# Kernel optimization log

Measured on AMD Instinct MI355X. Metric: run time of the kernel, lower is better.

Reference implementation:

```python
import jax, jax.numpy as jnp
import numpy as np

D_IN, D_HID, N_TOK = 2048, 8192, 8192

def _ternary(key, shape):
    # ternary {-1, 0, 1} weights stored as float32
    return jax.random.randint(key, shape, -1, 2).astype(jnp.float32)

def setup_inputs() -> dict:
    key = jax.random.key(0)
    kx, k1, k2, kh, k3 = jax.random.split(key, 5)
    return {
        "x": jax.random.normal(kx, (N_TOK, D_IN), dtype=jnp.float32),
        "W1": _ternary(k1, (D_HID, D_IN)),   # gate proj
        "W2": _ternary(k2, (D_HID, D_IN)),   # value proj
        "Wh": _ternary(kh, (D_HID, D_HID)),  # hidden layer (depth-1 == 1)
        "W3": _ternary(k3, (D_IN, D_HID)),   # output proj
        # per-layer dequant scales (scalar), ~1/sqrt(fan_in)
        "s1": jnp.float32(1.0 / np.sqrt(D_IN)),
        "s2": jnp.float32(1.0 / np.sqrt(D_IN)),
        "sh": jnp.float32(1.0 / np.sqrt(D_HID)),
        "s3": jnp.float32(1.0 / np.sqrt(D_HID)),
    }

def _tlin(x, W, s):
    # ternary packed linear: dequantized matmul, no bias
    return jnp.einsum('td,hd->th', x, W) * s

def reference(x, W1, W2, Wh, W3, s1, s2, sh, s3):
    h = jax.nn.silu(_tlin(x, W1, s1)) * _tlin(x, W2, s2)   # SwiGLU entry
    h = jax.nn.gelu(_tlin(h, Wh, sh), approximate=False)    # hidden block (depth-1)
    return _tlin(h, W3, s3)                                 # [N_TOK, D_IN]
```

## Files before the change

### kernel.cpp

```cpp
#include <hip/hip_runtime.h>
#include <hip/hip_bf16.h>
#include <stdint.h>

typedef __bf16 bf16;
typedef __bf16 bf16x8 __attribute__((ext_vector_type(8)));
typedef float f32x4 __attribute__((ext_vector_type(4)));

typedef uint32_t __attribute__((address_space(1))) * gptr_as1;
typedef uint32_t __attribute__((address_space(3))) * lptr_as3;

__device__ __forceinline__ void async16(const void* g, void* l) {
    __builtin_amdgcn_global_load_lds((gptr_as1)(uintptr_t)g,
                                     (lptr_as3)(uintptr_t)l,
                                     16, 0, 0);
}

__device__ __forceinline__ void bar() {
    asm volatile("" ::: "memory");
    __builtin_amdgcn_s_barrier();
    asm volatile("" ::: "memory");
}

__global__ void cvt_f32_bf16_kernel(const float* __restrict__ src,
                                    bf16* __restrict__ dst, int n8) {
    int i = blockIdx.x * blockDim.x + threadIdx.x;
    if (i >= n8) return;
    const float4* s = reinterpret_cast<const float4*>(src);
    float4 a = s[2 * (size_t)i], b = s[2 * (size_t)i + 1];
    bf16x8 v;
    v[0] = (bf16)a.x; v[1] = (bf16)a.y; v[2] = (bf16)a.z; v[3] = (bf16)a.w;
    v[4] = (bf16)b.x; v[5] = (bf16)b.y; v[6] = (bf16)b.z; v[7] = (bf16)b.w;
    *reinterpret_cast<bf16x8*>(dst + (size_t)i * 8) = v;
}

__global__ void cvt_ilv_kernel(const float* __restrict__ src,
                               bf16* __restrict__ dst, int n8, int sel) {
    int i = blockIdx.x * blockDim.x + threadIdx.x;
    if (i >= n8) return;
    const int row = i >> 8;
    const int c = i & 255;
    const int drow = ((row >> 4) << 5) + (sel << 4) + (row & 15);
    const float4* s = reinterpret_cast<const float4*>(src);
    float4 a = s[2 * (size_t)i], b = s[2 * (size_t)i + 1];
    bf16x8 v;
    v[0] = (bf16)a.x; v[1] = (bf16)a.y; v[2] = (bf16)a.z; v[3] = (bf16)a.w;
    v[4] = (bf16)b.x; v[5] = (bf16)b.y; v[6] = (bf16)b.z; v[7] = (bf16)b.w;
    *reinterpret_cast<bf16x8*>(dst + ((size_t)drow * 256 + c) * 8) = v;
}

template <int EPI, int K>
__global__ __launch_bounds__(256, 2)
void gemm2t(const bf16* __restrict__ A, const bf16* __restrict__ B,
            void* __restrict__ Cout, const float* __restrict__ s1p,
            const float* __restrict__ s2p, int N, int ldh) {
    __shared__ __align__(16) char sm[49152];

    const int tid = threadIdx.x;
    const int w = tid >> 6, l = tid & 63;
    const int wr = w >> 1, wc = w & 1;

    const int gx = gridDim.x;
    const int nwg = gx * (int)gridDim.y;
    const int orig = blockIdx.y * gx + blockIdx.x;
    const int wg = (orig & 7) * (nwg >> 3) + (orig >> 3);
    const int bm = wg / gx, bn = wg % gx;

    constexpr int NT = K / 32;

    f32x4 acc[8][4] = {};

    const int arow = bm * 256, brow = bn * 128;

    const int sr = l >> 2;
    const int sg = ((l & 3) ^ ((l >> 3) & 3)) << 4;
    const char* qa0 = (const char*)(A + (size_t)(arow +   0 + w * 16 + sr) * K) + sg;
    const char* qa1 = (const char*)(A + (size_t)(arow +  64 + w * 16 + sr) * K) + sg;
    const char* qa2 = (const char*)(A + (size_t)(arow + 128 + w * 16 + sr) * K) + sg;
    const char* qa3 = (const char*)(A + (size_t)(arow + 192 + w * 16 + sr) * K) + sg;
    const char* qb0 = (const char*)(B + (size_t)(brow +   0 + w * 16 + sr) * K) + sg;
    const char* qb1 = (const char*)(B + (size_t)(brow +  64 + w * 16 + sr) * K) + sg;
    const int ldw = w * 1024;

    auto STAGE_TILE = [&](int p) {
        char* ba = sm + p * 24576;
        char* bb = ba + 16384;
        async16(qa0, ba +     0 + ldw); async16(qa1, ba +  4096 + ldw);
        async16(qa2, ba +  8192 + ldw); async16(qa3, ba + 12288 + ldw);
        async16(qb0, bb +     0 + ldw); async16(qb1, bb +  4096 + ldw);
    };
    auto ADV = [&]() {
        qa0 += 64; qa1 += 64; qa2 += 64; qa3 += 64; qb0 += 64; qb1 += 64;
    };

    const int rlane = l & 15;
    const int chi = (l >> 4) << 4;

    STAGE_TILE(0);
    ADV();
    asm volatile("s_waitcnt vmcnt(0)" ::: "memory");
    bar();

#pragma unroll 1
    for (int kt = 0; kt < NT; ++kt) {
        if (kt + 1 < NT) { STAGE_TILE((kt + 1) & 1); ADV(); }
        const char* ba = sm + (kt & 1) * 24576;
        const char* bb = ba + 16384;

        bf16x8 av[8], bv[4];
#pragma unroll
        for (int i = 0; i < 8; ++i) {
            const int row = wr * 128 + i * 16 + rlane;
            av[i] = *reinterpret_cast<const bf16x8*>(
                ba + row * 64 + (chi ^ (((row >> 1) & 3) << 4)));
        }
#pragma unroll
        for (int j = 0; j < 4; ++j) {
            const int row = wc * 64 + j * 16 + rlane;
            bv[j] = *reinterpret_cast<const bf16x8*>(
                bb + row * 64 + (chi ^ (((row >> 1) & 3) << 4)));
        }
        asm volatile("s_waitcnt lgkmcnt(0)" ::: "memory");
        __builtin_amdgcn_sched_barrier(0);
        __builtin_amdgcn_s_setprio(1);
#pragma unroll
        for (int i = 0; i < 8; ++i)
#pragma unroll
            for (int j = 0; j < 4; ++j)
                acc[i][j] = __builtin_amdgcn_mfma_f32_16x16x32_bf16(av[i], bv[j], acc[i][j], 0, 0, 0);
        __builtin_amdgcn_s_setprio(0);
        asm volatile("s_waitcnt vmcnt(0)" ::: "memory");
        bar();
    }

    const float s1 = s1p[0];
    const int r0 = bm * 256 + wr * 128 + ((l >> 4) << 2);
    if constexpr (EPI == 2) {
        const float s2 = s2p[0];
        const int hcb = (bn * 4 + wc * 2) * 16 + rlane;
#pragma unroll
        for (int i = 0; i < 8; ++i)
#pragma unroll
            for (int jp = 0; jp < 2; ++jp)
#pragma unroll
                for (int q = 0; q < 4; ++q) {
                    float g = acc[i][2 * jp][q] * s1;
                    float v = acc[i][2 * jp + 1][q] * s2;
                    float sig = 1.0f / (1.0f + __expf(-g));
                    ((bf16*)Cout)[(size_t)(r0 + i * 16 + q) * ldh + hcb + jp * 16] =
                        (bf16)(g * sig * v);
                }
    } else {
        const int c0 = bn * 128 + wc * 64 + rlane;
#pragma unroll
        for (int i = 0; i < 8; ++i)
#pragma unroll
            for (int j = 0; j < 4; ++j)
#pragma unroll
                for (int q = 0; q < 4; ++q) {
                    float v = acc[i][j][q] * s1;
                    size_t idx = (size_t)(r0 + i * 16 + q) * N + (c0 + j * 16);
                    if constexpr (EPI == 0) {
                        float g = 0.5f * v * (1.0f + erff(v * 0.70710678118654752f));
                        ((bf16*)Cout)[idx] = (bf16)g;
                    } else {
                        ((float*)Cout)[idx] = v;
                    }
                }
    }
}

template <int EPI, int K>
__global__ __launch_bounds__(512, 1)
void gemm8p(const bf16* __restrict__ A, const bf16* __restrict__ B,
            void* __restrict__ Cout, const float* __restrict__ s1p,
            const float* __restrict__ s2p, int N, int ldh) {
    __shared__ __align__(16) char sm[131072];

    const int tid = threadIdx.x;
    const int w = tid >> 6, l = tid & 63;
    const int wr = w >> 2, wc = w & 3;

    const int gx = gridDim.x;
    const int nwg = gx * (int)gridDim.y;
    const int orig = blockIdx.y * gx + blockIdx.x;
    const int wg = (orig & 7) * (nwg >> 3) + (orig >> 3);
    const int bm = wg / gx, bn = wg % gx;

    constexpr int NT = K / 64;

    f32x4 acc[8][4] = {};

    char* const bufA0 = sm;
    char* const bufB0 = sm + 32768;
    char* const bufA1 = sm + 65536;
    char* const bufB1 = sm + 98304;
    const int arow = bm * 256, brow = bn * 256;

    const int srow_in = l >> 3;
    const int scolb = ((l & 7) ^ srow_in) << 4;
    auto STAGE = [&](char* ldsT, const bf16* g, int grow0, int kt, int r0) {
        const int rr = r0 + w * 8 + srow_in;
        const char* gp = (const char*)(g + (size_t)(grow0 + rr) * K + kt * 64) + scolb;
        async16(gp, ldsT + r0 * 128 + w * 1024);
    };

    const int rlane = l & 15;
    const int chi = (l >> 4) << 4;
    const int sw = (rlane & 7) << 4;
    const int ksd = (rlane & 4) ? -64 : 64;
    const int offA = (wr * 128 + rlane) * 128 + (chi ^ sw);
    const int offB = (wc * 64 + rlane) * 128 + (chi ^ sw);
    const char* const pA0  = bufA0 + offA;  const char* const pA0k = pA0 + ksd;
    const char* const pB0  = bufB0 + offB;  const char* const pB0k = pB0 + ksd;
    const char* const pA1  = bufA1 + offA;  const char* const pA1k = pA1 + ksd;
    const char* const pB1  = bufB1 + offB;  const char* const pB1k = pB1 + ksd;

    STAGE(bufA0, A, arow, 0, 0);   STAGE(bufA0, A, arow, 0, 128);
    STAGE(bufB0, B, brow, 0, 0);   STAGE(bufB0, B, brow, 0, 64);
    STAGE(bufB0, B, brow, 0, 128); STAGE(bufB0, B, brow, 0, 192);
    STAGE(bufA0, A, arow, 0, 64);  STAGE(bufA0, A, arow, 0, 192);
    STAGE(bufA1, A, arow, 1, 0);   STAGE(bufA1, A, arow, 1, 128);
    STAGE(bufB1, B, brow, 1, 0);   STAGE(bufB1, B, brow, 1, 64);
    STAGE(bufB1, B, brow, 1, 128); STAGE(bufB1, B, brow, 1, 192);
    asm volatile("s_waitcnt vmcnt(6)" ::: "memory");
    bar();

    auto body = [&](int kt, char* cA, char* cB, char* nA,
                    const char* pa, const char* pak,
                    const char* pb, const char* pbk) {
        bf16x8 ae[4], ao[4], bv[4];
#pragma unroll
        for (int i = 0; i < 4; ++i)
            ae[i] = *reinterpret_cast<const bf16x8*>(pa + i * 2048);
#pragma unroll
        for (int j = 0; j < 4; ++j)
            bv[j] = *reinterpret_cast<const bf16x8*>(pb + j * 2048);
        if (kt + 1 < NT) { STAGE(nA, A, arow, kt + 1, 64); STAGE(nA, A, arow, kt + 1, 192); }
        bar();
        asm volatile("s_waitcnt lgkmcnt(0)" ::: "memory");
        __builtin_amdgcn_sched_barrier(0);
        __builtin_amdgcn_s_setprio(1);
#pragma unroll
        for (int i = 0; i < 4; ++i)
#pragma unroll
            for (int j = 0; j < 4; ++j)
                acc[i][j] = __builtin_amdgcn_mfma_f32_16x16x32_bf16(ae[i], bv[j], acc[i][j], 0, 0, 0);
        __builtin_amdgcn_s_setprio(0);
        bar();
#pragma unroll
        for (int i = 0; i < 4; ++i)
            ao[i] = *reinterpret_cast<const bf16x8*>(pa + 8192 + i * 2048);
        bar();
        asm volatile("s_waitcnt lgkmcnt(0)" ::: "memory");
        __builtin_amdgcn_sched_barrier(0);
        __builtin_amdgcn_s_setprio(1);
#pragma unroll
        for (int i = 0; i < 4; ++i)
#pragma unroll
            for (int j = 0; j < 4; ++j)
                acc[4 + i][j] = __builtin_amdgcn_mfma_f32_16x16x32_bf16(ao[i], bv[j], acc[4 + i][j], 0, 0, 0);
        __builtin_amdgcn_s_setprio(0);
        bar();
#pragma unroll
        for (int i = 0; i < 4; ++i)
            ae[i] = *reinterpret_cast<const bf16x8*>(pak + i * 2048);
#pragma unroll
        for (int j = 0; j < 4; ++j)
            bv[j] = *reinterpret_cast<const bf16x8*>(pbk + j * 2048);
        if (kt + 2 < NT) { STAGE(cB, B, brow, kt + 2, 0); STAGE(cB, B, brow, kt + 2, 64); }
        bar();
        asm volatile("s_waitcnt lgkmcnt(0)" ::: "memory");
        __builtin_amdgcn_sched_barrier(0);
        __builtin_amdgcn_s_setprio(1);
#pragma unroll
        for (int i = 0; i < 4; ++i)
#pragma unroll
            for (int j = 0; j < 4; ++j)
                acc[i][j] = __builtin_amdgcn_mfma_f32_16x16x32_bf16(ae[i], bv[j], acc[i][j], 0, 0, 0);
        __builtin_amdgcn_s_setprio(0);
        bar();
#pragma unroll
        for (int i = 0; i < 4; ++i)
            ao[i] = *reinterpret_cast<const bf16x8*>(pak + 8192 + i * 2048);
        if (kt + 2 < NT) {
            STAGE(cB, B, brow, kt + 2, 128); STAGE(cB, B, brow, kt + 2, 192);
            STAGE(cA, A, arow, kt + 2, 0);   STAGE(cA, A, arow, kt + 2, 128);
        }
        bar();
        asm volatile("s_waitcnt lgkmcnt(0)" ::: "memory");
        __builtin_amdgcn_sched_barrier(0);
        __builtin_amdgcn_s_setprio(1);
#pragma unroll
        for (int i = 0; i < 4; ++i)
#pragma unroll
            for (int j = 0; j < 4; ++j)
                acc[4 + i][j] = __builtin_amdgcn_mfma_f32_16x16x32_bf16(ao[i], bv[j], acc[4 + i][j], 0, 0, 0);
        __builtin_amdgcn_s_setprio(0);
        if (kt == NT - 2) { asm volatile("s_waitcnt vmcnt(0)" ::: "memory"); }
        else              { asm volatile("s_waitcnt vmcnt(6)" ::: "memory"); }
        bar();
    };

#pragma unroll 1
    for (int kt = 0; kt < NT; kt += 2) {
        body(kt,     bufA0, bufB0, bufA1, pA0, pA0k, pB0, pB0k);
        body(kt + 1, bufA1, bufB1, bufA0, pA1, pA1k, pB1, pB1k);
    }

    const float s1 = s1p[0];
    const int r0 = bm * 256 + wr * 128 + ((l >> 4) << 2);
    if constexpr (EPI == 2) {
        const float s2 = s2p[0];
        const int hcb = (bn * 8 + wc * 2) * 16 + rlane;
#pragma unroll
        for (int i = 0; i < 8; ++i)
#pragma unroll
            for (int jp = 0; jp < 2; ++jp)
#pragma unroll
                for (int q = 0; q < 4; ++q) {
                    float g = acc[i][2 * jp][q] * s1;
                    float v = acc[i][2 * jp + 1][q] * s2;
                    float sig = 1.0f / (1.0f + __expf(-g));
                    ((bf16*)Cout)[(size_t)(r0 + i * 16 + q) * ldh + hcb + jp * 16] =
                        (bf16)(g * sig * v);
                }
    } else {
        const int c0 = bn * 256 + wc * 64 + rlane;
#pragma unroll
        for (int i = 0; i < 8; ++i)
#pragma unroll
            for (int j = 0; j < 4; ++j)
#pragma unroll
                for (int q = 0; q < 4; ++q) {
                    float v = acc[i][j][q] * s1;
                    size_t idx = (size_t)(r0 + i * 16 + q) * N + (c0 + j * 16);
                    if constexpr (EPI == 0) {
                        float g = 0.5f * v * (1.0f + erff(v * 0.70710678118654752f));
                        ((bf16*)Cout)[idx] = (bf16)g;
                    } else {
                        ((float*)Cout)[idx] = v;
                    }
                }
    }
}

extern "C" void kernel_launch(void* const* d_in, const int* in_sizes, int n_in,
                              void* d_out, int out_size, void* d_ws, size_t ws_size,
                              hipStream_t stream) {
    constexpr int NTOK = 8192, DIN = 2048, DHID = 8192;

    const float* x  = (const float*)d_in[0];
    const float* W1 = (const float*)d_in[1];
    const float* W2 = (const float*)d_in[2];
    const float* Wh = (const float*)d_in[3];
    const float* W3 = (const float*)d_in[4];
    const float* s1 = (const float*)d_in[5];
    const float* s2 = (const float*)d_in[6];
    const float* sh = (const float*)d_in[7];
    const float* s3 = (const float*)d_in[8];
    float* out = (float*)d_out;

    char* ws = (char*)d_ws;
    size_t off = 0;
    bf16* xb   = (bf16*)(ws + off); off += (size_t)NTOK * DIN * 2;
    bf16* w12b = (bf16*)(ws + off); off += (size_t)2 * DHID * DIN * 2;
    bf16* w3b  = (bf16*)(ws + off); off += (size_t)DIN * DHID * 2;
    bf16* whb  = (bf16*)(ws + off); off += (size_t)DHID * DHID * 2;
    bf16* h1   = (bf16*)(ws + off); off += (size_t)NTOK * DHID * 2;
    bf16* h2   = (bf16*)(ws + off); off += (size_t)NTOK * DHID * 2;
    if (ws_size < off) return;

    auto cvt = [&](const float* s, bf16* d, size_t n) {
        int n8 = (int)(n / 8);
        cvt_f32_bf16_kernel<<<(n8 + 255) / 256, 256, 0, stream>>>(s, d, n8);
    };
    cvt(x,  xb,  (size_t)NTOK * DIN);
    cvt(Wh, whb, (size_t)DHID * DHID);
    cvt(W3, w3b, (size_t)DIN * DHID);
    {
        int n8 = (int)((size_t)DHID * DIN / 8);
        cvt_ilv_kernel<<<(n8 + 255) / 256, 256, 0, stream>>>(W1, w12b, n8, 0);
        cvt_ilv_kernel<<<(n8 + 255) / 256, 256, 0, stream>>>(W2, w12b, n8, 1);
    }

    gemm8p<2, DIN><<<dim3(2 * DHID / 256, NTOK / 256), 512, 0, stream>>>(
        xb, w12b, h1, s1, s2, 2 * DHID, DHID);
    gemm2t<0, DHID><<<dim3(DHID / 128, NTOK / 256), 256, 0, stream>>>(
        h1, whb, h2, sh, sh, DHID, DHID);
    gemm8p<1, DHID><<<dim3(DIN / 256, NTOK / 256), 512, 0, stream>>>(
        h2, w3b, out, s3, s3, DIN, DIN);
}
```

Measured before the change: 1.890 ms.

## Replace hidden GEMM with 256x256 four-stage pipelined kernel; relax gemm8p barriers

The hidden-layer GEMM moves from a 256-thread, 256x128-tile double-buffered kernel to a 512-thread, 256x256-tile kernel. It stages tiles in pairs into a four-buffer 128KB LDS ring, so global loads run further ahead of the MFMA work and each loaded tile feeds more MFMAs. The gemm8p body also drops several intermediate barriers and lgkmcnt waits and issues its async stages earlier, aiming to cut synchronisation stalls. The larger tile lowers occupancy to one block per CU and raises register pressure. Removing the waits relies on compiler-inserted counters and may risk LDS races with the async writes.

```diff
diff --git a/kernel.cpp b/kernel.cpp
--- a/kernel.cpp
+++ b/kernel.cpp
@@ -49,15 +49,15 @@
 }
 
 template <int EPI, int K>
-__global__ __launch_bounds__(256, 2)
-void gemm2t(const bf16* __restrict__ A, const bf16* __restrict__ B,
-            void* __restrict__ Cout, const float* __restrict__ s1p,
-            const float* __restrict__ s2p, int N, int ldh) {
-    __shared__ __align__(16) char sm[49152];
+__global__ __launch_bounds__(512, 1)
+void gemm4sp(const bf16* __restrict__ A, const bf16* __restrict__ B,
+             void* __restrict__ Cout, const float* __restrict__ s1p,
+             const float* __restrict__ s2p, int N, int ldh) {
+    __shared__ __align__(16) char sm[131072];
 
     const int tid = threadIdx.x;
     const int w = tid >> 6, l = tid & 63;
-    const int wr = w >> 1, wc = w & 1;
+    const int wr = w >> 2, wc = w & 3;
 
     const int gx = gridDim.x;
     const int nwg = gx * (int)gridDim.y;
@@ -69,74 +69,88 @@
 
     f32x4 acc[8][4] = {};
 
-    const int arow = bm * 256, brow = bn * 128;
+    const int arow = bm * 256, brow = bn * 256;
 
     const int sr = l >> 2;
     const int sg = ((l & 3) ^ ((l >> 3) & 3)) << 4;
     const char* qa0 = (const char*)(A + (size_t)(arow +   0 + w * 16 + sr) * K) + sg;
-    const char* qa1 = (const char*)(A + (size_t)(arow +  64 + w * 16 + sr) * K) + sg;
-    const char* qa2 = (const char*)(A + (size_t)(arow + 128 + w * 16 + sr) * K) + sg;
-    const char* qa3 = (const char*)(A + (size_t)(arow + 192 + w * 16 + sr) * K) + sg;
+    const char* qa1 = (const char*)(A + (size_t)(arow + 128 + w * 16 + sr) * K) + sg;
     const char* qb0 = (const char*)(B + (size_t)(brow +   0 + w * 16 + sr) * K) + sg;
-    const char* qb1 = (const char*)(B + (size_t)(brow +  64 + w * 16 + sr) * K) + sg;
+    const char* qb1 = (const char*)(B + (size_t)(brow + 128 + w * 16 + sr) * K) + sg;
     const int ldw = w * 1024;
-
-    auto STAGE_TILE = [&](int p) {
-        char* ba = sm + p * 24576;
-        char* bb = ba + 16384;
-        async16(qa0, ba +     0 + ldw); async16(qa1, ba +  4096 + ldw);
-        async16(qa2, ba +  8192 + ldw); async16(qa3, ba + 12288 + ldw);
-        async16(qb0, bb +     0 + ldw); async16(qb1, bb +  4096 + ldw);
-    };
-    auto ADV = [&]() {
-        qa0 += 64; qa1 += 64; qa2 += 64; qa3 += 64; qb0 += 64; qb1 += 64;
+    auto STAGE_PAIR = [&](char* se, char* so) {
+        async16(qa0,      se +     0 + ldw);
+        async16(qa1,      se +  8192 + ldw);
+        async16(qb0,      se + 16384 + ldw);
+        async16(qb1,      se + 24576 + ldw);
+        async16(qa0 + 64, so +     0 + ldw);
+        async16(qa1 + 64, so +  8192 + ldw);
+        async16(qb0 + 64, so + 16384 + ldw);
+        async16(qb1 + 64, so + 24576 + ldw);
+        qa0 += 128; qa1 += 128; qb0 += 128; qb1 += 128;
     };
 
     const int rlane = l & 15;
     const int chi = (l >> 4) << 4;
-
-    STAGE_TILE(0);
-    ADV();
-    asm volatile("s_waitcnt vmcnt(0)" ::: "memory");
+    const int swz = ((rlane >> 1) & 3) << 4;
+    const int offA = (wr * 128 + rlane) * 64 + (chi ^ swz);
+    const int offB = (wc * 64 + rlane) * 64 + (chi ^ swz);
+    const char* const pA0 = sm +      0 + offA;
+    const char* const pA1 = sm +  32768 + offA;
+    const char* const pA2 = sm +  65536 + offA;
+    const char* const pA3 = sm +  98304 + offA;
+    const char* const pB0 = sm +  16384 + offB;
+    const char* const pB1 = sm +  49152 + offB;
+    const char* const pB2 = sm +  81920 + offB;
+    const char* const pB3 = sm + 114688 + offB;
+
+    STAGE_PAIR(sm, sm + 32768);
+    asm volatile("s_waitcnt vmcnt(4)" ::: "memory");
     bar();
 
+    auto compute = [&](const char* pa, const char* pb) {
+        bf16x8 bv[4], av[8];
+#pragma unroll
+        for (int j = 0; j < 4; ++j)
+            bv[j] = *reinterpret_cast<const bf16x8*>(pb + j * 1024);
+#pragma unroll
+        for (int i = 0; i < 8; ++i)
+            av[i] = *reinterpret_cast<const bf16x8*>(pa + i * 1024);
+        __builtin_amdgcn_s_setprio(1);
+#pragma unroll
+        for (int i = 0; i < 8; ++i)
+#pragma unroll
+            for (int j = 0; j < 4; ++j)
+                acc[i][j] = __builtin_amdgcn_mfma_f32_16x16x32_bf16(av[i], bv[j], acc[i][j], 0, 0, 0);
+        __builtin_amdgcn_s_setprio(0);
+    };
+
+    auto body_even = [&](int kt, const char* pa, const char* pb, char* se, char* so) {
+        if (kt + 2 < NT) STAGE_PAIR(se, so);
+        compute(pa, pb);
+        if (kt + 2 < NT) { asm volatile("s_waitcnt vmcnt(8)" ::: "memory"); }
+        else             { asm volatile("s_waitcnt vmcnt(0)" ::: "memory"); }
+        bar();
+    };
+    auto body_odd = [&](int kt, const char* pa, const char* pb) {
+        compute(pa, pb);
+        if (kt + 1 < NT) { asm volatile("s_waitcnt vmcnt(4)" ::: "memory"); }
+        bar();
+    };
+
 #pragma unroll 1
-    for (int kt = 0; kt < NT; ++kt) {
-        if (kt + 1 < NT) { STAGE_TILE((kt + 1) & 1); ADV(); }
-        const char* ba = sm + (kt & 1) * 24576;
-        const char* bb = ba + 16384;
-
-        bf16x8 av[8], bv[4];
-#pragma unroll
-        for (int i = 0; i < 8; ++i) {
-            const int row = wr * 128 + i * 16 + rlane;
-            av[i] = *reinterpret_cast<const bf16x8*>(
-                ba + row * 64 + (chi ^ (((row >> 1) & 3) << 4)));
-        }
-#pragma unroll
-        for (int j = 0; j < 4; ++j) {
-            const int row = wc * 64 + j * 16 + rlane;
-            bv[j] = *reinterpret_cast<const bf16x8*>(
-                bb + row * 64 + (chi ^ (((row >> 1) & 3) << 4)));
-        }
-        asm volatile("s_waitcnt lgkmcnt(0)" ::: "memory");
-        __builtin_amdgcn_sched_barrier(0);
-        __builtin_amdgcn_s_setprio(1);
-#pragma unroll
-        for (int i = 0; i < 8; ++i)
-#pragma unroll
-            for (int j = 0; j < 4; ++j)
-                acc[i][j] = __builtin_amdgcn_mfma_f32_16x16x32_bf16(av[i], bv[j], acc[i][j], 0, 0, 0);
-        __builtin_amdgcn_s_setprio(0);
-        asm volatile("s_waitcnt vmcnt(0)" ::: "memory");
-        bar();
+    for (int kt = 0; kt < NT; kt += 4) {
+        body_even(kt + 0, pA0, pB0, sm + 65536, sm + 98304);
+        body_odd (kt + 1, pA1, pB1);
+        body_even(kt + 2, pA2, pB2, sm, sm + 32768);
+        body_odd (kt + 3, pA3, pB3);
     }
 
     const float s1 = s1p[0];
     const int r0 = bm * 256 + wr * 128 + ((l >> 4) << 2);
     if constexpr (EPI == 2) {
         const float s2 = s2p[0];
-        const int hcb = (bn * 4 + wc * 2) * 16 + rlane;
+        const int hcb = (bn * 8 + wc * 2) * 16 + rlane;
 #pragma unroll
         for (int i = 0; i < 8; ++i)
 #pragma unroll
@@ -150,7 +164,7 @@
                         (bf16)(g * sig * v);
                 }
     } else {
-        const int c0 = bn * 128 + wc * 64 + rlane;
+        const int c0 = bn * 256 + wc * 64 + rlane;
 #pragma unroll
         for (int i = 0; i < 8; ++i)
 #pragma unroll
@@ -229,16 +243,13 @@
                     const char* pa, const char* pak,
                     const char* pb, const char* pbk) {
         bf16x8 ae[4], ao[4], bv[4];
+        if (kt + 1 < NT) { STAGE(nA, A, arow, kt + 1, 64); STAGE(nA, A, arow, kt + 1, 192); }
 #pragma unroll
         for (int i = 0; i < 4; ++i)
             ae[i] = *reinterpret_cast<const bf16x8*>(pa + i * 2048);
 #pragma unroll
         for (int j = 0; j < 4; ++j)
             bv[j] = *reinterpret_cast<const bf16x8*>(pb + j * 2048);
-        if (kt + 1 < NT) { STAGE(nA, A, arow, kt + 1, 64); STAGE(nA, A, arow, kt + 1, 192); }
-        bar();
-        asm volatile("s_waitcnt lgkmcnt(0)" ::: "memory");
-        __builtin_amdgcn_sched_barrier(0);
         __builtin_amdgcn_s_setprio(1);
 #pragma unroll
         for (int i = 0; i < 4; ++i)
@@ -250,9 +261,6 @@
 #pragma unroll
         for (int i = 0; i < 4; ++i)
             ao[i] = *reinterpret_cast<const bf16x8*>(pa + 8192 + i * 2048);
-        bar();
-        asm volatile("s_waitcnt lgkmcnt(0)" ::: "memory");
-        __builtin_amdgcn_sched_barrier(0);
         __builtin_amdgcn_s_setprio(1);
 #pragma unroll
         for (int i = 0; i < 4; ++i)
@@ -267,10 +275,6 @@
 #pragma unroll
         for (int j = 0; j < 4; ++j)
             bv[j] = *reinterpret_cast<const bf16x8*>(pbk + j * 2048);
-        if (kt + 2 < NT) { STAGE(cB, B, brow, kt + 2, 0); STAGE(cB, B, brow, kt + 2, 64); }
-        bar();
-        asm volatile("s_waitcnt lgkmcnt(0)" ::: "memory");
-        __builtin_amdgcn_sched_barrier(0);
         __builtin_amdgcn_s_setprio(1);
 #pragma unroll
         for (int i = 0; i < 4; ++i)
@@ -279,16 +283,14 @@
                 acc[i][j] = __builtin_amdgcn_mfma_f32_16x16x32_bf16(ae[i], bv[j], acc[i][j], 0, 0, 0);
         __builtin_amdgcn_s_setprio(0);
         bar();
-#pragma unroll
-        for (int i = 0; i < 4; ++i)
-            ao[i] = *reinterpret_cast<const bf16x8*>(pak + 8192 + i * 2048);
         if (kt + 2 < NT) {
+            STAGE(cB, B, brow, kt + 2, 0);   STAGE(cB, B, brow, kt + 2, 64);
             STAGE(cB, B, brow, kt + 2, 128); STAGE(cB, B, brow, kt + 2, 192);
             STAGE(cA, A, arow, kt + 2, 0);   STAGE(cA, A, arow, kt + 2, 128);
         }
-        bar();
-        asm volatile("s_waitcnt lgkmcnt(0)" ::: "memory");
-        __builtin_amdgcn_sched_barrier(0);
+#pragma unroll
+        for (int i = 0; i < 4; ++i)
+            ao[i] = *reinterpret_cast<const bf16x8*>(pak + 8192 + i * 2048);
         __builtin_amdgcn_s_setprio(1);
 #pragma unroll
         for (int i = 0; i < 4; ++i)
@@ -385,7 +387,7 @@
 
     gemm8p<2, DIN><<<dim3(2 * DHID / 256, NTOK / 256), 512, 0, stream>>>(
         xb, w12b, h1, s1, s2, 2 * DHID, DHID);
-    gemm2t<0, DHID><<<dim3(DHID / 128, NTOK / 256), 256, 0, stream>>>(
+    gemm4sp<0, DHID><<<dim3(DHID / 256, NTOK / 256), 512, 0, stream>>>(
         h1, whb, h2, sh, sh, DHID, DHID);
     gemm8p<1, DHID><<<dim3(DIN / 256, NTOK / 256), 512, 0, stream>>>(
         h2, w3b, out, s3, s3, DIN, DIN);
```

Result: slower. 1.968 ms (+4.1%).
